# Performance work log

Measured on AMD Instinct MI355X. Metric: run time of the kernel, lower is better.

The kernel has to match this reference:

```python
import jax, jax.numpy as jnp
import numpy as np

TOPK = 2
RENORMALIZE = True

T, H, I, E = 2048, 2048, 5632, 8  # tokens, hidden, intermediate, experts


def setup_inputs() -> dict:
    key = jax.random.key(0)
    k1, k2, k3, k4 = jax.random.split(key, 4)
    x = jax.random.normal(k1, (T, H), dtype=jnp.float32)
    gating_output = jax.random.normal(k2, (T, E), dtype=jnp.float32)
    # gate_up_proj: concat of gate [E,I,H] and up [E,I,H] along dim 1 -> [E,2I,H]
    w1 = jax.random.normal(k3, (E, 2 * I, H), dtype=jnp.float32) * 0.02
    # down_proj: [E, H, I]
    w2 = jax.random.normal(k4, (E, H, I), dtype=jnp.float32) * 0.02
    return {"x": x, "gating_output": gating_output, "w1": w1, "w2": w2}


def _route(gating_output):
    # standard (non-grouped) top-k softmax routing, renormalized
    probs = jax.nn.softmax(gating_output, axis=-1)            # [T, E]
    topk_w, topk_idx = jax.lax.top_k(probs, TOPK)             # [T, K]
    if RENORMALIZE:
        topk_w = topk_w / jnp.sum(topk_w, axis=-1, keepdims=True)
    t = gating_output.shape[0]
    route = jnp.zeros((t, gating_output.shape[1]), dtype=topk_w.dtype)
    route = route.at[jnp.arange(t)[:, None], topk_idx].set(topk_w)  # [T, E]
    return route


def reference(x, gating_output, w1, w2):
    route = _route(gating_output)                             # [T, E]
    inter = w2.shape[-1]
    out = jnp.zeros_like(x)
    # loop over small fixed expert count; each iter is dense GEMM work
    for e in range(w1.shape[0]):
        gu = x @ w1[e].T                                      # [T, 2I]
        h = jax.nn.silu(gu[:, :inter]) * gu[:, inter:]        # SwiGLU  [T, I]
        out = out + (h @ w2[e].T) * route[:, e:e + 1]         # [T, H]
    return out
```

## Files before the change

kernel.cpp:

```cpp
#include <hip/hip_runtime.h>
#include <hip/hip_bf16.h>


#define TT 2048
#define HH 2048
#define II 5632
#define NE 8

using f32x4  = __attribute__((ext_vector_type(4))) float;
using bf16x8 = __attribute__((ext_vector_type(8))) short;

__device__ __forceinline__ uint32_t bfbits(float f) {
    __hip_bfloat16 h = __float2bfloat16(f);
    unsigned short u;
    __builtin_memcpy(&u, &h, 2);
    return (uint32_t)u;
}
__device__ __forceinline__ uint32_t pk2(float a, float b) {
    return bfbits(a) | (bfbits(b) << 16);
}
__device__ __forceinline__ uint4 pk8(const float4& a, const float4& b) {
    uint4 r;
    r.x = pk2(a.x, a.y); r.y = pk2(a.z, a.w);
    r.z = pk2(b.x, b.y); r.w = pk2(b.z, b.w);
    return r;
}
__device__ __forceinline__ void gl16(const void* g, void* l) {
    __builtin_amdgcn_global_load_lds(
        (const __attribute__((address_space(1))) unsigned int*)g,
        (__attribute__((address_space(3))) unsigned int*)l, 16, 0, 0);
}

__global__ void cvt_x(const float* __restrict__ x, __hip_bfloat16* __restrict__ xb) {
    const int i = (blockIdx.x * 256 + threadIdx.x) * 8;
    float4 a = *(const float4*)(x + i);
    float4 b = *(const float4*)(x + i + 4);
    *(uint4*)(xb + i) = pk8(a, b);
}

__global__ void route_topk(const float* __restrict__ gating,
                           int* __restrict__ tk_idx, float* __restrict__ tk_w) {
    int t = blockIdx.x * 256 + threadIdx.x;
    if (t >= TT) return;
    float g[NE];
#pragma unroll
    for (int e = 0; e < NE; e++) g[e] = gating[t * NE + e];
    int i0 = 0; float b0 = g[0];
#pragma unroll
    for (int e = 1; e < NE; e++) if (g[e] > b0) { b0 = g[e]; i0 = e; }
    int i1 = (i0 == 0) ? 1 : 0; float b1 = g[i1];
#pragma unroll
    for (int e = 0; e < NE; e++) if (e != i0 && g[e] > b1) { b1 = g[e]; i1 = e; }
    float ex = expf(b1 - b0);
    float w0 = 1.f / (1.f + ex);
    float w1 = ex / (1.f + ex);
    tk_idx[2 * t] = i0; tk_idx[2 * t + 1] = i1;
    tk_w[2 * t] = w0;  tk_w[2 * t + 1] = w1;
}

__global__ void build_lists(const int* __restrict__ tk_idx, const float* __restrict__ tk_w,
                            int* __restrict__ list_tok, int* __restrict__ inv,
                            int* __restrict__ counts) {
    const int e = blockIdx.x;
    const int tid = threadIdx.x;
    int flag[8];
    int cnt = 0;
#pragma unroll
    for (int j = 0; j < 8; j++) {
        int t = tid * 8 + j;
        int f = -1;
        if (tk_idx[2 * t] == e) f = 0;
        else if (tk_idx[2 * t + 1] == e) f = 1;
        flag[j] = f;
        cnt += (f >= 0) ? 1 : 0;
    }
    __shared__ int s[256];
    s[tid] = cnt;
    __syncthreads();
    for (int d = 1; d < 256; d <<= 1) {
        int v = (tid >= d) ? s[tid - d] : 0;
        __syncthreads();
        s[tid] += v;
        __syncthreads();
    }
    int pos = s[tid] - cnt;
#pragma unroll
    for (int j = 0; j < 8; j++) {
        if (flag[j] >= 0) {
            int t = tid * 8 + j;
            list_tok[e * TT + pos] = t;
            inv[2 * t + flag[j]] = e * TT + pos;
            pos++;
        }
    }
    if (tid == 255) counts[e] = s[255];
}

__global__ __launch_bounds__(512, 4) void gemm1_swiglu(
    const __hip_bfloat16* __restrict__ xb, const float* __restrict__ w1,
    const int* __restrict__ list_tok, const int* __restrict__ counts,
    __hip_bfloat16* __restrict__ hbuf) {
    const int e = blockIdx.y >> 3;
    const int mt = blockIdx.y & 7;
    const int cnt = counts[e];
    const int row0 = mt * 256;
    if (row0 >= cnt) return;
    int off = 0;
#pragma unroll
    for (int i = 0; i < NE; i++) if (i < e) off += counts[i];
    const int valid = min(256, cnt - row0);
    const int n0 = blockIdx.x * 64;
    const int tid = threadIdx.x;
    const int w = tid >> 6, l = tid & 63;

    __shared__ uint4 As[2 * 1024];
    __shared__ uint4 Bs[2][512];

    const char *aSrc0, *aSrc1;
    {
        int r0 = w * 16 + (l >> 2);
        int r1 = r0 + 128;
        int t0 = list_tok[e * TT + row0 + min(r0, valid - 1)];
        int t1 = list_tok[e * TT + row0 + min(r1, valid - 1)];
        int s0 = (l & 3) ^ ((r0 >> 1) & 3);
        int s1 = (l & 3) ^ ((r1 >> 1) & 3);
        aSrc0 = (const char*)(xb + (size_t)t0 * HH + s0 * 8);
        aSrc1 = (const char*)(xb + (size_t)t1 * HH + s1 * 8);
    }
    auto STAGEA = [&](int kt, int b) {
        char* ab = (char*)As + b * 16384 + w * 1024;
        gl16(aSrc0 + (size_t)kt * 64, ab);
        gl16(aSrc1 + (size_t)kt * 64, ab + 8192);
    };

    const int br = tid >> 2, bu2 = tid & 3;
    const float* bSrc;
    {
        const float* base = w1 + (size_t)e * (2 * II) * HH;
        int r = (br < 64) ? (n0 + br) : (II + n0 + (br - 64));
        bSrc = base + (size_t)r * HH + bu2 * 8;
    }
    const int bwi = br * 4 + (bu2 ^ ((br >> 1) & 3));

    float4 rBa, rBb;
    auto LOADB = [&](int kt) {
        const int k = kt * 32;
        rBa = *(const float4*)(bSrc + k); rBb = *(const float4*)(bSrc + k + 4);
    };
    auto STOREB = [&](int b) { Bs[b][bwi] = pk8(rBa, rBb); };

    const int wm = w >> 1, wn = w & 1;
    const int l15 = l & 15, ks = l >> 4;
    int aidx[4], bgidx[2], buidx[2];
#pragma unroll
    for (int m = 0; m < 4; m++) { int r = wm * 64 + m * 16 + l15; aidx[m] = r * 4 + (ks ^ ((r >> 1) & 3)); }
#pragma unroll
    for (int n = 0; n < 2; n++) {
        int cg = wn * 32 + n * 16 + l15;
        int cu = cg + 64;
        bgidx[n] = cg * 4 + (ks ^ ((cg >> 1) & 3));
        buidx[n] = cu * 4 + (ks ^ ((cu >> 1) & 3));
    }

    f32x4 accg[4][2], accu[4][2];
#pragma unroll
    for (int m = 0; m < 4; m++)
#pragma unroll
        for (int n = 0; n < 2; n++) { accg[m][n] = 0; accu[m][n] = 0; }

    STAGEA(0, 0); LOADB(0); STOREB(0);
    __syncthreads();
    const int KT = HH / 32;
#pragma unroll 2
    for (int kt = 0; kt < KT; ++kt) {
        const int cur = kt & 1;
        if (kt + 1 < KT) {
            STAGEA(kt + 1, cur ^ 1);
            LOADB(kt + 1);
        }
        bf16x8 gf[2], uf[2];
#pragma unroll
        for (int n = 0; n < 2; n++) {
            uint4 t = Bs[cur][bgidx[n]]; gf[n] = __builtin_bit_cast(bf16x8, t);
            uint4 t2 = Bs[cur][buidx[n]]; uf[n] = __builtin_bit_cast(bf16x8, t2);
        }
        const uint4* Ab = As + cur * 1024;
#pragma unroll
        for (int m = 0; m < 4; m++) {
            uint4 t = Ab[aidx[m]];
            bf16x8 af = __builtin_bit_cast(bf16x8, t);
#pragma unroll
            for (int n = 0; n < 2; n++) {
                accg[m][n] = __builtin_amdgcn_mfma_f32_16x16x32_bf16(af, gf[n], accg[m][n], 0, 0, 0);
                accu[m][n] = __builtin_amdgcn_mfma_f32_16x16x32_bf16(af, uf[n], accu[m][n], 0, 0, 0);
            }
        }
        if (kt + 1 < KT) STOREB(cur ^ 1);
        __syncthreads();
    }

#pragma unroll
    for (int m = 0; m < 4; m++) {
#pragma unroll
        for (int r = 0; r < 4; r++) {
            const int lr = wm * 64 + m * 16 + ks * 4 + r;
            if (lr < valid) {
                __hip_bfloat16* hrow = hbuf + (size_t)(off + row0 + lr) * II;
#pragma unroll
                for (int n = 0; n < 2; n++) {
                    const int col = n0 + wn * 32 + n * 16 + l15;
                    float g = accg[m][n][r], u = accu[m][n][r];
                    float h = g / (1.f + __expf(-g)) * u;
                    hrow[col] = __float2bfloat16(h);
                }
            }
        }
    }
}

__global__ __launch_bounds__(512, 4) void gemm2_rows(
    const __hip_bfloat16* __restrict__ hbuf, const float* __restrict__ w2,
    const int* __restrict__ counts, float* __restrict__ gbuf) {
    const int e = blockIdx.y >> 3;
    const int mt = blockIdx.y & 7;
    const int cnt = counts[e];
    const int row0 = mt * 256;
    if (row0 >= cnt) return;
    int off = 0;
#pragma unroll
    for (int i = 0; i < NE; i++) if (i < e) off += counts[i];
    const int valid = min(256, cnt - row0);
    const int n0 = blockIdx.x * 128;
    const int tid = threadIdx.x;
    const int w = tid >> 6, l = tid & 63;

    __shared__ uint4 As[2 * 1024];
    __shared__ uint4 Bs[2][512];

    const char *aSrc0, *aSrc1;
    {
        int r0 = w * 16 + (l >> 2);
        int r1 = r0 + 128;
        int s0 = (l & 3) ^ ((r0 >> 1) & 3);
        int s1 = (l & 3) ^ ((r1 >> 1) & 3);
        aSrc0 = (const char*)(hbuf + (size_t)(off + row0 + min(r0, valid - 1)) * II + s0 * 8);
        aSrc1 = (const char*)(hbuf + (size_t)(off + row0 + min(r1, valid - 1)) * II + s1 * 8);
    }
    auto STAGEA = [&](int kt, int b) {
        char* ab = (char*)As + b * 16384 + w * 1024;
        gl16(aSrc0 + (size_t)kt * 64, ab);
        gl16(aSrc1 + (size_t)kt * 64, ab + 8192);
    };

    const int br = tid >> 2, bu2 = tid & 3;
    const float* bSrc = w2 + (size_t)e * HH * II + (size_t)(n0 + br) * II + bu2 * 8;
    const int bwi = br * 4 + (bu2 ^ ((br >> 1) & 3));

    float4 rBa, rBb;
    auto LOADB = [&](int kt) {
        const int k = kt * 32;
        rBa = *(const float4*)(bSrc + k); rBb = *(const float4*)(bSrc + k + 4);
    };
    auto STOREB = [&](int b) { Bs[b][bwi] = pk8(rBa, rBb); };

    const int wm = w >> 2, wn = w & 3;
    const int l15 = l & 15, ks = l >> 4;
    int aidx[8], bidx[2];
#pragma unroll
    for (int m = 0; m < 8; m++) { int r = wm * 128 + m * 16 + l15; aidx[m] = r * 4 + (ks ^ ((r >> 1) & 3)); }
#pragma unroll
    for (int n = 0; n < 2; n++) { int c = wn * 32 + n * 16 + l15; bidx[n] = c * 4 + (ks ^ ((c >> 1) & 3)); }

    f32x4 acc[8][2];
#pragma unroll
    for (int m = 0; m < 8; m++)
#pragma unroll
        for (int n = 0; n < 2; n++) acc[m][n] = 0;

    STAGEA(0, 0); LOADB(0); STOREB(0);
    __syncthreads();
    const int KT = II / 32;
#pragma unroll 2
    for (int kt = 0; kt < KT; ++kt) {
        const int cur = kt & 1;
        if (kt + 1 < KT) {
            STAGEA(kt + 1, cur ^ 1);
            LOADB(kt + 1);
        }
        bf16x8 bf[2];
#pragma unroll
        for (int n = 0; n < 2; n++) { uint4 t = Bs[cur][bidx[n]]; bf[n] = __builtin_bit_cast(bf16x8, t); }
        const uint4* Ab = As + cur * 1024;
#pragma unroll
        for (int m = 0; m < 8; m++) {
            uint4 t = Ab[aidx[m]];
            bf16x8 af = __builtin_bit_cast(bf16x8, t);
#pragma unroll
            for (int n = 0; n < 2; n++)
                acc[m][n] = __builtin_amdgcn_mfma_f32_16x16x32_bf16(af, bf[n], acc[m][n], 0, 0, 0);
        }
        if (kt + 1 < KT) STOREB(cur ^ 1);
        __syncthreads();
    }

#pragma unroll
    for (int m = 0; m < 8; m++) {
#pragma unroll
        for (int r = 0; r < 4; r++) {
            const int lr = wm * 128 + m * 16 + ks * 4 + r;
            if (lr < valid) {
                float* orow = gbuf + (size_t)(off + row0 + lr) * HH;
#pragma unroll
                for (int n = 0; n < 2; n++) {
                    const int col = n0 + wn * 32 + n * 16 + l15;
                    orow[col] = acc[m][n][r];
                }
            }
        }
    }
}

__global__ void combine(const float* __restrict__ gbuf, const int* __restrict__ inv,
                        const float* __restrict__ tk_w, const int* __restrict__ counts,
                        float* __restrict__ out) {
    const int idx = blockIdx.x * 256 + threadIdx.x;
    const int t = idx >> 8;
    const int c = (idx & 255) * 8;
    int offs[NE];
    {
        int s = 0;
#pragma unroll
        for (int e = 0; e < NE; e++) { offs[e] = s; s += counts[e]; }
    }
    const int i0 = inv[2 * t], i1 = inv[2 * t + 1];
    const float w0 = tk_w[2 * t], w1 = tk_w[2 * t + 1];
    const float* g0 = gbuf + (size_t)(offs[i0 >> 11] + (i0 & 2047)) * HH + c;
    const float* g1 = gbuf + (size_t)(offs[i1 >> 11] + (i1 & 2047)) * HH + c;
    float4 a0 = *(const float4*)(g0);
    float4 a1 = *(const float4*)(g0 + 4);
    float4 b0 = *(const float4*)(g1);
    float4 b1 = *(const float4*)(g1 + 4);
    float4 o0, o1;
    o0.x = w0 * a0.x + w1 * b0.x; o0.y = w0 * a0.y + w1 * b0.y;
    o0.z = w0 * a0.z + w1 * b0.z; o0.w = w0 * a0.w + w1 * b0.w;
    o1.x = w0 * a1.x + w1 * b1.x; o1.y = w0 * a1.y + w1 * b1.y;
    o1.z = w0 * a1.z + w1 * b1.z; o1.w = w0 * a1.w + w1 * b1.w;
    float* op = out + (size_t)t * HH + c;
    *(float4*)(op) = o0;
    *(float4*)(op + 4) = o1;
}

extern "C" void kernel_launch(void* const* d_in, const int* in_sizes, int n_in,
                              void* d_out, int out_size, void* d_ws, size_t ws_size,
                              hipStream_t stream) {
    const float* x      = (const float*)d_in[0];
    const float* gating = (const float*)d_in[1];
    const float* w1     = (const float*)d_in[2];
    const float* w2     = (const float*)d_in[3];
    float* out = (float*)d_out;
    char* ws = (char*)d_ws;

    int*   list_tok = (int*)(ws + 0);
    int*   inv      = (int*)(ws + (64 << 10));
    int*   counts   = (int*)(ws + (96 << 10));
    int*   tk_idx   = (int*)(ws + (100 << 10));
    float* tk_w     = (float*)(ws + (116 << 10));
    __hip_bfloat16* hbuf = (__hip_bfloat16*)(ws + (1 << 20));
    float* gbuf = (float*)(ws + (size_t)(64 << 20));

    __hip_bfloat16* xb = (__hip_bfloat16*)d_out;

    route_topk<<<TT / 256, 256, 0, stream>>>(gating, tk_idx, tk_w);
    build_lists<<<NE, 256, 0, stream>>>(tk_idx, tk_w, list_tok, inv, counts);
    cvt_x<<<TT * HH / (256 * 8), 256, 0, stream>>>(x, xb);
    gemm1_swiglu<<<dim3(II / 64, NE * 8), 512, 0, stream>>>(xb, w1, list_tok, counts, hbuf);
    gemm2_rows<<<dim3(HH / 128, NE * 8), 512, 0, stream>>>(hbuf, w2, counts, gbuf);
    combine<<<TT * HH / (256 * 8), 256, 0, stream>>>(gbuf, inv, tk_w, counts, out);
}
```

Before: 675.2 us.

## Deepen GEMM pipelines to triple-buffered A with manual vmcnt waits

Both expert GEMM kernels now keep three LDS stages for the A tile and issue loads two iterations ahead. Each iteration stores the B tile fetched on the previous one, and full __syncthreads is replaced by explicit lgkmcnt/vmcnt waits plus s_barrier, so async global-to-LDS loads can stay in flight across iterations. The aim is to hide global memory latency behind MFMA work. The cost is more LDS per block, which may lower occupancy, and vmcnt(4) counting that assumes a fixed number of outstanding loads, which is fragile.

```diff
diff --git a/kernel.cpp b/kernel.cpp
--- a/kernel.cpp
+++ b/kernel.cpp
@@ -30,6 +30,11 @@
         (const __attribute__((address_space(1))) unsigned int*)g,
         (__attribute__((address_space(3))) unsigned int*)l, 16, 0, 0);
 }
+
+#define VMW4() asm volatile("s_waitcnt vmcnt(4)" ::: "memory")
+#define VMW0() asm volatile("s_waitcnt vmcnt(0)" ::: "memory")
+#define LGKM0() asm volatile("s_waitcnt lgkmcnt(0)" ::: "memory")
+#define BARR() __builtin_amdgcn_s_barrier()
 
 __global__ void cvt_x(const float* __restrict__ x, __hip_bfloat16* __restrict__ xb) {
     const int i = (blockIdx.x * 256 + threadIdx.x) * 8;
@@ -113,7 +118,7 @@
     const int tid = threadIdx.x;
     const int w = tid >> 6, l = tid & 63;
 
-    __shared__ uint4 As[2 * 1024];
+    __shared__ uint4 As[3 * 1024];
     __shared__ uint4 Bs[2][512];
 
     const char *aSrc0, *aSrc1;
@@ -168,15 +173,22 @@
 #pragma unroll
         for (int n = 0; n < 2; n++) { accg[m][n] = 0; accu[m][n] = 0; }
 
-    STAGEA(0, 0); LOADB(0); STOREB(0);
-    __syncthreads();
     const int KT = HH / 32;
-#pragma unroll 2
+    STAGEA(0, 0); STAGEA(1, 1); LOADB(0);
+    VMW0();
+    STOREB(0);
+    LOADB(1);
+    LGKM0();
+    BARR();
+
+    int abR = 0;
     for (int kt = 0; kt < KT; ++kt) {
         const int cur = kt & 1;
-        if (kt + 1 < KT) {
-            STAGEA(kt + 1, cur ^ 1);
-            LOADB(kt + 1);
+        if (kt + 1 < KT) STOREB(cur ^ 1);
+        if (kt + 2 < KT) {
+            LOADB(kt + 2);
+            int abW = (abR == 0) ? 2 : abR - 1;
+            STAGEA(kt + 2, abW);
         }
         bf16x8 gf[2], uf[2];
 #pragma unroll
@@ -184,7 +196,7 @@
             uint4 t = Bs[cur][bgidx[n]]; gf[n] = __builtin_bit_cast(bf16x8, t);
             uint4 t2 = Bs[cur][buidx[n]]; uf[n] = __builtin_bit_cast(bf16x8, t2);
         }
-        const uint4* Ab = As + cur * 1024;
+        const uint4* Ab = As + abR * 1024;
 #pragma unroll
         for (int m = 0; m < 4; m++) {
             uint4 t = Ab[aidx[m]];
@@ -195,8 +207,12 @@
                 accu[m][n] = __builtin_amdgcn_mfma_f32_16x16x32_bf16(af, uf[n], accu[m][n], 0, 0, 0);
             }
         }
-        if (kt + 1 < KT) STOREB(cur ^ 1);
-        __syncthreads();
+        if (kt + 1 < KT) {
+            LGKM0();
+            if (kt + 2 < KT) VMW4(); else VMW0();
+            BARR();
+        }
+        abR = (abR == 2) ? 0 : abR + 1;
     }
 
 #pragma unroll
@@ -234,7 +250,7 @@
     const int tid = threadIdx.x;
     const int w = tid >> 6, l = tid & 63;
 
-    __shared__ uint4 As[2 * 1024];
+    __shared__ uint4 As[3 * 1024];
     __shared__ uint4 Bs[2][512];
 
     const char *aSrc0, *aSrc1;
@@ -277,20 +293,27 @@
 #pragma unroll
         for (int n = 0; n < 2; n++) acc[m][n] = 0;
 
-    STAGEA(0, 0); LOADB(0); STOREB(0);
-    __syncthreads();
     const int KT = II / 32;
-#pragma unroll 2
+    STAGEA(0, 0); STAGEA(1, 1); LOADB(0);
+    VMW0();
+    STOREB(0);
+    LOADB(1);
+    LGKM0();
+    BARR();
+
+    int abR = 0;
     for (int kt = 0; kt < KT; ++kt) {
         const int cur = kt & 1;
-        if (kt + 1 < KT) {
-            STAGEA(kt + 1, cur ^ 1);
-            LOADB(kt + 1);
+        if (kt + 1 < KT) STOREB(cur ^ 1);
+        if (kt + 2 < KT) {
+            LOADB(kt + 2);
+            int abW = (abR == 0) ? 2 : abR - 1;
+            STAGEA(kt + 2, abW);
         }
         bf16x8 bf[2];
 #pragma unroll
         for (int n = 0; n < 2; n++) { uint4 t = Bs[cur][bidx[n]]; bf[n] = __builtin_bit_cast(bf16x8, t); }
-        const uint4* Ab = As + cur * 1024;
+        const uint4* Ab = As + abR * 1024;
 #pragma unroll
         for (int m = 0; m < 8; m++) {
             uint4 t = Ab[aidx[m]];
@@ -299,8 +322,12 @@
             for (int n = 0; n < 2; n++)
                 acc[m][n] = __builtin_amdgcn_mfma_f32_16x16x32_bf16(af, bf[n], acc[m][n], 0, 0, 0);
         }
-        if (kt + 1 < KT) STOREB(cur ^ 1);
-        __syncthreads();
+        if (kt + 1 < KT) {
+            LGKM0();
+            if (kt + 2 < KT) VMW4(); else VMW0();
+            BARR();
+        }
+        abR = (abR == 2) ? 0 : abR + 1;
     }
 
 #pragma unroll
```

New measurement: 675.2 us. Within noise of the previous version (-0.0%).
